# Optimization experiments

Measured on AMD Instinct MI355X. Metric: run time of the kernel, lower is better.

## Reference

```python
import jax, jax.numpy as jnp
import numpy as np

B, IN, H, O, DEPTH = 16384, 64, 128, 32, 4


def _xavier(k, shape):
    fan_in, fan_out = shape[-2], shape[-1]
    lim = float(np.sqrt(6.0 / (fan_in + fan_out)))
    return jax.random.uniform(k, shape, jnp.float32, -lim, lim)


def _gru(x, h, wi, bi, wh, bh):
    # x: [B,1,O], h: [B,1,H]; wi: [3,O,H], wh: [3,H,H]
    r = jax.nn.sigmoid(x @ wi[0] + bi[0] + h @ wh[0] + bh[0])
    z = jax.nn.sigmoid(x @ wi[1] + bi[1] + h @ wh[1] + bh[1])
    n = jnp.tanh(x @ wi[2] + bi[2] + r * (h @ wh[2] + bh[2]))
    return (1.0 - z) * n + z * h


def setup_inputs() -> dict:
    key = jax.random.key(0)
    ks = jax.random.split(key, 10)
    return {
        "z": jax.random.normal(ks[0], (B, 1, IN), jnp.float32),
        "z2h_w": _xavier(ks[1], (IN, H)), "z2h_b": jnp.zeros((H,), jnp.float32),
        "h2o_w": _xavier(ks[2], (H, O)), "h2o_b": jnp.zeros((O,), jnp.float32),
        "gru_a_wi": _xavier(ks[3], (3, O, H)), "gru_a_bi": jnp.zeros((3, H), jnp.float32),
        "gru_a_wh": _xavier(ks[4], (3, H, H)), "gru_a_bh": jnp.zeros((3, H), jnp.float32),
        "gru_f_wi": _xavier(ks[5], (3, O, H)), "gru_f_bi": jnp.zeros((3, H), jnp.float32),
        "gru_f_wh": _xavier(ks[6], (3, H, H)), "gru_f_bh": jnp.zeros((3, H), jnp.float32),
        "u_a_w": _xavier(ks[7], (H, H)), "u_a_b": jnp.zeros((H,), jnp.float32),
        "u_f_w": _xavier(ks[8], (H, H)), "u_f_b": jnp.zeros((H,), jnp.float32),
        "depth": DEPTH,
    }


def reference(z, z2h_w, z2h_b, h2o_w, h2o_b,
              gru_a_wi, gru_a_bi, gru_a_wh, gru_a_bh,
              gru_f_wi, gru_f_bi, gru_f_wh, gru_f_bh,
              u_a_w, u_a_b, u_f_w, u_f_b, depth):
    preds = []

    def node(h_a, d):
        # h_a: [B,1,H] incoming (ancestral) hidden for this node
        pred = h_a @ h2o_w + h2o_b            # [B,1,O] symbol logits
        probs = jax.nn.softmax(pred, axis=2)
        preds.append(pred)
        h_ai = _gru(probs, h_a, gru_a_wi, gru_a_bi, gru_a_wh, gru_a_bh)
        if d > 0:
            # first child: gets ancestral hidden directly
            probs_f = node(h_ai, d - 1)
            # second child: fraternal GRU over first child's root probs,
            # combined with this node's incoming hidden via u_f / u_a
            h_f = _gru(probs_f, h_ai, gru_f_wi, gru_f_bi, gru_f_wh, gru_f_bh)
            h2 = jnp.tanh(h_f @ u_f_w + u_f_b + h_a @ u_a_w + u_a_b)
            node(h2, d - 1)
        return probs

    hidden = z @ z2h_w + z2h_b                # [B,1,H]
    node(hidden, int(depth))
    return jnp.stack(preds, axis=0)           # [n_nodes, B, 1, O] preorder
```

## Files before the change

kernel.cpp:

```cpp
#include <hip/hip_runtime.h>
#include <cstddef>


#define BB   16384
#define HH   128
#define OO   32
#define ROWS 64

typedef __attribute__((ext_vector_type(8))) short bf8;
typedef __attribute__((ext_vector_type(4))) float f4;

#define MFMA(a, b, c) __builtin_amdgcn_mfma_f32_16x16x32_bf16(a, b, c, 0, 0, 0)

#define PW_Z2H 0
#define PW_AWI 8192
#define PW_AWH 20480
#define PW_FWI 69632
#define PW_FWH 81920
#define PW_UA  131072
#define PW_UF  147456
#define PW_H2O 163840
#define PW_END 167936

#define SH   136
#define PSLD 40

#define BA_RZ  0
#define BA_BH2 256
#define BA_BI2 384
#define BF_RZ  512
#define BF_BH2 768
#define BF_BI2 896
#define BU     1024
#define BZ2H   1152
#define BH2O   1280
#define BIAS_N 1312

__device__ __forceinline__ short f2bf(float f) {
  union { float f; unsigned u; } v; v.f = f;
  unsigned r = v.u + 0x7fff + ((v.u >> 16) & 1);
  return (short)(r >> 16);
}
__device__ __forceinline__ float bf2f(short h) {
  union { unsigned u; float f; } v;
  v.u = ((unsigned)(unsigned short)h) << 16;
  return v.f;
}
__device__ __forceinline__ float rcp_(float x) { return __builtin_amdgcn_rcpf(x); }
__device__ __forceinline__ float sigmoidf_(float x) { return rcp_(1.0f + __expf(-x)); }
__device__ __forceinline__ float tanhf_(float x) {
  float ax = fabsf(x), e = __expf(-2.0f * ax);
  float t = (1.0f - e) * rcp_(1.0f + e);
  return x >= 0.0f ? t : -t;
}

template <int K, int N>
__device__ __forceinline__ void repack_one(const float* __restrict__ W,
                                           short* __restrict__ P, int idx) {
  const int KC = K / 32;
  const int j = idx & 7, lane = (idx >> 3) & 63, rest = idx >> 9;
  const int kc = rest % KC, nt = rest / KC;
  const int k = kc * 32 + ((lane >> 4) << 3) + j;
  const int n = nt * 16 + (lane & 15);
  P[idx] = f2bf(W[(size_t)k * N + n]);
}

__global__ __launch_bounds__(256) void k_repack(
    const float* __restrict__ z2hw, const float* __restrict__ awi,
    const float* __restrict__ awh, const float* __restrict__ fwi,
    const float* __restrict__ fwh, const float* __restrict__ uaw,
    const float* __restrict__ ufw, const float* __restrict__ h2ow,
    short* __restrict__ ws) {
  const int t = blockIdx.x * 256 + threadIdx.x;
  if (t < PW_AWI)        repack_one<64, 128>(z2hw, ws + PW_Z2H, t - PW_Z2H);
  else if (t < PW_AWH)   repack_one<96, 128>(awi, ws + PW_AWI, t - PW_AWI);
  else if (t < PW_FWI)   repack_one<384, 128>(awh, ws + PW_AWH, t - PW_AWH);
  else if (t < PW_FWH)   repack_one<96, 128>(fwi, ws + PW_FWI, t - PW_FWI);
  else if (t < PW_UA)    repack_one<384, 128>(fwh, ws + PW_FWH, t - PW_FWH);
  else if (t < PW_UF)    repack_one<128, 128>(uaw, ws + PW_UA, t - PW_UA);
  else if (t < PW_H2O)   repack_one<128, 128>(ufw, ws + PW_UF, t - PW_UF);
  else if (t < PW_END)   repack_one<128, 32>(h2ow, ws + PW_H2O, t - PW_H2O);
}

__device__ __forceinline__ void store_slice(const f4* hv, short* dst, int lane, int w) {
  const int l15 = lane & 15, q = lane >> 4;
#pragma unroll
  for (int rt = 0; rt < 4; ++rt)
#pragma unroll
    for (int j = 0; j < 4; ++j)
      dst[(rt * 16 + q * 4 + j) * SH + w * 16 + l15] = f2bf(hv[rt][j]);
}

__device__ __forceinline__ void gru_slice(const short* xs, const short* hsrc,
                                          const short* wiP, const short* whP,
                                          const float* brz, const float* bh2v,
                                          const float* bi2v,
                                          int lane, int w, f4* hv) {
  const int l15 = lane & 15, q = lane >> 4;
  const int col = w * 16 + l15;
  bf8 ax[4], ah[4][4];
#pragma unroll
  for (int rt = 0; rt < 4; ++rt) {
    ax[rt] = *(const bf8*)(xs + (rt * 16 + l15) * PSLD + q * 8);
#pragma unroll
    for (int c = 0; c < 4; ++c)
      ah[rt][c] = *(const bf8*)(hsrc + (rt * 16 + l15) * SH + c * 32 + q * 8);
  }
  const bf8* wi = (const bf8*)wiP;
  const bf8* wh = (const bf8*)whP;
  f4 t2[4], rg[4];
  {
    const float b = bh2v[col];
#pragma unroll
    for (int rt = 0; rt < 4; ++rt) t2[rt] = (f4){b, b, b, b};
  }
  {
    bf8 W[4];
#pragma unroll
    for (int c = 0; c < 4; ++c) W[c] = wh[(w * 12 + 8 + c) * 64 + lane];
#pragma unroll
    for (int c = 0; c < 4; ++c)
#pragma unroll
      for (int rt = 0; rt < 4; ++rt) t2[rt] = MFMA(ah[rt][c], W[c], t2[rt]);
  }
  {
    const float b = brz[col];
#pragma unroll
    for (int rt = 0; rt < 4; ++rt) rg[rt] = (f4){b, b, b, b};
  }
  {
    bf8 Wx = wi[(w * 3 + 0) * 64 + lane];
    bf8 W[4];
#pragma unroll
    for (int c = 0; c < 4; ++c) W[c] = wh[(w * 12 + 0 + c) * 64 + lane];
#pragma unroll
    for (int rt = 0; rt < 4; ++rt) rg[rt] = MFMA(ax[rt], Wx, rg[rt]);
#pragma unroll
    for (int c = 0; c < 4; ++c)
#pragma unroll
      for (int rt = 0; rt < 4; ++rt) rg[rt] = MFMA(ah[rt][c], W[c], rg[rt]);
  }
#pragma unroll
  for (int k = 0; k < 4; ++k)
#pragma unroll
    for (int j = 0; j < 4; ++j) t2[k][j] *= sigmoidf_(rg[k][j]);
  {
    const float b = bi2v[col];
#pragma unroll
    for (int k = 0; k < 4; ++k)
#pragma unroll
      for (int j = 0; j < 4; ++j) t2[k][j] += b;
  }
  {
    bf8 Wx = wi[(w * 3 + 2) * 64 + lane];
#pragma unroll
    for (int rt = 0; rt < 4; ++rt) t2[rt] = MFMA(ax[rt], Wx, t2[rt]);
  }
  {
    const float b = brz[128 + col];
#pragma unroll
    for (int rt = 0; rt < 4; ++rt) rg[rt] = (f4){b, b, b, b};
  }
  {
    bf8 Wx = wi[(w * 3 + 1) * 64 + lane];
    bf8 W[4];
#pragma unroll
    for (int c = 0; c < 4; ++c) W[c] = wh[(w * 12 + 4 + c) * 64 + lane];
#pragma unroll
    for (int rt = 0; rt < 4; ++rt) rg[rt] = MFMA(ax[rt], Wx, rg[rt]);
#pragma unroll
    for (int c = 0; c < 4; ++c)
#pragma unroll
      for (int rt = 0; rt < 4; ++rt) rg[rt] = MFMA(ah[rt][c], W[c], rg[rt]);
  }
#pragma unroll
  for (int rt = 0; rt < 4; ++rt)
#pragma unroll
    for (int j = 0; j < 4; ++j) {
      const float hc = bf2f(hsrc[(rt * 16 + q * 4 + j) * SH + col]);
      const float zz = sigmoidf_(rg[rt][j]);
      const float nn = tanhf_(t2[rt][j]);
      hv[rt][j] = nn + zz * (hc - nn);
    }
}

__device__ __forceinline__ void pred_node16(const short* hsrc,
                                            const short* h2oP,
                                            const float* bo,
                                            float* spred, short* pdst,
                                            int lane, int w) {
  const int l15 = lane & 15, q = lane >> 4;
  bf8 a[4];
#pragma unroll
  for (int c = 0; c < 4; ++c)
    a[c] = *(const bf8*)(hsrc + (w * 16 + l15) * SH + c * 32 + q * 8);
  const bf8* bw = (const bf8*)h2oP;
  bf8 W[8];
#pragma unroll
  for (int f = 0; f < 8; ++f) W[f] = bw[f * 64 + lane];
  f4 p[2];
#pragma unroll
  for (int nt = 0; nt < 2; ++nt) {
    const float b = bo[nt * 16 + l15];
    f4 acc = (f4){b, b, b, b};
#pragma unroll
    for (int c = 0; c < 4; ++c) acc = MFMA(a[c], W[nt * 4 + c], acc);
    p[nt] = acc;
  }
#pragma unroll
  for (int j = 0; j < 4; ++j) {
    const float v0 = p[0][j], v1 = p[1][j];
    float mx = fmaxf(v0, v1);
#pragma unroll
    for (int s = 1; s < 16; s <<= 1) mx = fmaxf(mx, __shfl_xor(mx, s));
    const float e0 = __expf(v0 - mx), e1 = __expf(v1 - mx);
    float ss = e0 + e1;
#pragma unroll
    for (int s = 1; s < 16; s <<= 1) ss += __shfl_xor(ss, s);
    const float inv = rcp_(ss);
    const int row = w * 16 + q * 4 + j;
    spred[row * 32 + l15] = v0;
    spred[row * 32 + 16 + l15] = v1;
    pdst[row * PSLD + l15] = f2bf(e0 * inv);
    pdst[row * PSLD + 16 + l15] = f2bf(e1 * inv);
  }
}

__device__ const unsigned char d_TYPE[31] =
    {0,1,1,1,1,2,2,1,2,2,1,1,2,2,1,2,2,1,1,1,2,2,1,2,2,1,1,2,2,1,2};
__device__ const unsigned char d_LVL[31] =
    {0,1,2,3,4,4,3,4,4,2,3,4,4,3,4,4,1,2,3,4,4,3,4,4,2,3,4,4,3,4,4};

__global__ __launch_bounds__(512, 2) void k_tree(
    const float* __restrict__ zf, const short* __restrict__ pw,
    const float* __restrict__ z2hb, const float* __restrict__ abi,
    const float* __restrict__ abh, const float* __restrict__ fbi,
    const float* __restrict__ fbh, const float* __restrict__ uab,
    const float* __restrict__ ufb, const float* __restrict__ h2ob,
    float* __restrict__ out) {
  __shared__ __align__(16) short hstk[5 * ROWS * SH];
  __shared__ __align__(16) short hfb[ROWS * SH];
  __shared__ __align__(16) short pstk[5 * ROWS * PSLD];
  __shared__ float bias[BIAS_N];
  float* spred = (float*)hfb;
  const int lane = threadIdx.x & 63;
  const int w = threadIdx.x >> 6;
  const int l15 = lane & 15, q = lane >> 4;
  const int col = w * 16 + l15;
  const int r0 = blockIdx.x * ROWS;

  for (int t = threadIdx.x; t < BIAS_N; t += 512) {
    float v;
    if (t < 256)       v = abi[t] + abh[t];
    else if (t < 384)  v = abh[t];
    else if (t < 512)  v = abi[t - 128];
    else if (t < 768)  v = fbi[t - 512] + fbh[t - 512];
    else if (t < 896)  v = fbh[t - 512];
    else if (t < 1024) v = fbi[t - 640];
    else if (t < 1152) v = uab[t - 1024] + ufb[t - 1024];
    else if (t < 1280) v = z2hb[t - 1152];
    else               v = h2ob[t - 1280];
    bias[t] = v;
  }
  __syncthreads();

  {
    const bf8* wz = (const bf8*)(pw + PW_Z2H);
    const bf8 W0 = wz[(w * 2 + 0) * 64 + lane];
    const bf8 W1 = wz[(w * 2 + 1) * 64 + lane];
    const float b = bias[BZ2H + col];
    f4 hv[4];
#pragma unroll
    for (int rt = 0; rt < 4; ++rt) {
      const float* zr = zf + (size_t)(r0 + rt * 16 + l15) * 64 + q * 8;
      union { short s[8]; bf8 v; } A0, A1;
      {
        const f4 x0 = *(const f4*)zr, x1 = *(const f4*)(zr + 4);
#pragma unroll
        for (int j = 0; j < 4; ++j) { A0.s[j] = f2bf(x0[j]); A0.s[4 + j] = f2bf(x1[j]); }
        const f4 y0 = *(const f4*)(zr + 32), y1 = *(const f4*)(zr + 36);
#pragma unroll
        for (int j = 0; j < 4; ++j) { A1.s[j] = f2bf(y0[j]); A1.s[4 + j] = f2bf(y1[j]); }
      }
      f4 acc = (f4){b, b, b, b};
      acc = MFMA(A0.v, W0, acc);
      acc = MFMA(A1.v, W1, acc);
      hv[rt] = acc;
    }
    store_slice(hv, hstk, lane, w);
  }
  __syncthreads();

#pragma unroll 1
  for (int i = 0; i < 31; ++i) {
    const int t = d_TYPE[i];
    const int L = d_LVL[i];
    short* hcur = hstk + L * ROWS * SH;
    short* pcur = pstk + L * ROWS * PSLD;

    if (t == 2) {
      f4 hf[4];
      gru_slice(pcur, hcur, pw + PW_FWI, pw + PW_FWH,
                bias + BF_RZ, bias + BF_BH2, bias + BF_BI2, lane, w, hf);
      store_slice(hf, hfb, lane, w);
      __syncthreads();
      const short* hpar = hstk + (L - 1) * ROWS * SH;
      const bf8* uf = (const bf8*)(pw + PW_UF);
      const bf8* ua = (const bf8*)(pw + PW_UA);
      bf8 Wf[4], Wa[4];
#pragma unroll
      for (int c = 0; c < 4; ++c) {
        Wf[c] = uf[(w * 4 + c) * 64 + lane];
        Wa[c] = ua[(w * 4 + c) * 64 + lane];
      }
      const float b = bias[BU + col];
      f4 hv[4];
#pragma unroll
      for (int rt = 0; rt < 4; ++rt) {
        f4 acc = (f4){b, b, b, b};
#pragma unroll
        for (int c = 0; c < 4; ++c) {
          const bf8 af = *(const bf8*)(hfb + (rt * 16 + l15) * SH + c * 32 + q * 8);
          const bf8 ap = *(const bf8*)(hpar + (rt * 16 + l15) * SH + c * 32 + q * 8);
          acc = MFMA(af, Wf[c], acc);
          acc = MFMA(ap, Wa[c], acc);
        }
#pragma unroll
        for (int j = 0; j < 4; ++j) acc[j] = tanhf_(acc[j]);
        hv[rt] = acc;
      }
      store_slice(hv, hcur, lane, w);
      __syncthreads();
    }

    if (w < 4)
      pred_node16(hcur, pw + PW_H2O, bias + BH2O, spred, pcur, lane, w);
    __syncthreads();

    {
      const f4 v = *(const f4*)(spred + threadIdx.x * 4);
      __builtin_nontemporal_store(
          v, (f4*)(out + (size_t)i * BB * OO + (size_t)r0 * OO) + threadIdx.x);
    }

    if (L < 4) {
      f4 hv[4];
      gru_slice(pcur, hcur, pw + PW_AWI, pw + PW_AWH,
                bias + BA_RZ, bias + BA_BH2, bias + BA_BI2, lane, w, hv);
      store_slice(hv, hstk + (L + 1) * ROWS * SH, lane, w);
    }
    __syncthreads();
  }
}

extern "C" void kernel_launch(void* const* d_in, const int* in_sizes, int n_in,
                              void* d_out, int out_size, void* d_ws, size_t ws_size,
                              hipStream_t stream) {
  const float* z    = (const float*)d_in[0];
  const float* z2hw = (const float*)d_in[1];
  const float* z2hb = (const float*)d_in[2];
  const float* h2ow = (const float*)d_in[3];
  const float* h2ob = (const float*)d_in[4];
  const float* awi  = (const float*)d_in[5];
  const float* abi  = (const float*)d_in[6];
  const float* awh  = (const float*)d_in[7];
  const float* abh  = (const float*)d_in[8];
  const float* fwi  = (const float*)d_in[9];
  const float* fbi  = (const float*)d_in[10];
  const float* fwh  = (const float*)d_in[11];
  const float* fbh  = (const float*)d_in[12];
  const float* uaw  = (const float*)d_in[13];
  const float* uab  = (const float*)d_in[14];
  const float* ufw  = (const float*)d_in[15];
  const float* ufb  = (const float*)d_in[16];

  float* out = (float*)d_out;
  short* ws  = (short*)d_ws;

  k_repack<<<(PW_END + 255) / 256, 256, 0, stream>>>(
      z2hw, awi, awh, fwi, fwh, uaw, ufw, h2ow, ws);

  k_tree<<<BB / ROWS, 512, 0, stream>>>(
      z, ws, z2hb, abi, abh, fbi, fbh, uab, ufb, h2ob, out);
}
```

Measured before the change: 270.6 us.

## Inline pred node with direct stores, drop softmax max, vectorize repack

The pred/softmax step is inlined into the tree kernel. Logits now go straight to global memory, so the shared staging buffer and the later copy-out pass are gone. The softmax skips the max-subtraction shuffle reduction, and tanh uses a shorter formula; both rely on the inputs being bounded and risk overflow for large values. The repack kernel now has each thread write eight bf16 values as one vector store, and the final barrier only runs when a GRU step follows.

```diff
diff --git a/kernel.cpp b/kernel.cpp
--- a/kernel.cpp
+++ b/kernel.cpp
@@ -49,20 +49,22 @@
 __device__ __forceinline__ float rcp_(float x) { return __builtin_amdgcn_rcpf(x); }
 __device__ __forceinline__ float sigmoidf_(float x) { return rcp_(1.0f + __expf(-x)); }
 __device__ __forceinline__ float tanhf_(float x) {
-  float ax = fabsf(x), e = __expf(-2.0f * ax);
-  float t = (1.0f - e) * rcp_(1.0f + e);
-  return x >= 0.0f ? t : -t;
+  const float e = __expf(2.0f * x);
+  return 1.0f - 2.0f * rcp_(e + 1.0f);
 }
 
 template <int K, int N>
-__device__ __forceinline__ void repack_one(const float* __restrict__ W,
-                                           short* __restrict__ P, int idx) {
+__device__ __forceinline__ void repack8(const float* __restrict__ W,
+                                        short* __restrict__ P, int t) {
   const int KC = K / 32;
-  const int j = idx & 7, lane = (idx >> 3) & 63, rest = idx >> 9;
+  const int lane = t & 63, rest = t >> 6;
   const int kc = rest % KC, nt = rest / KC;
-  const int k = kc * 32 + ((lane >> 4) << 3) + j;
+  const int k0 = kc * 32 + ((lane >> 4) << 3);
   const int n = nt * 16 + (lane & 15);
-  P[idx] = f2bf(W[(size_t)k * N + n]);
+  union { short s[8]; bf8 v; } u;
+#pragma unroll
+  for (int j = 0; j < 8; ++j) u.s[j] = f2bf(W[(size_t)(k0 + j) * N + n]);
+  *(bf8*)(P + (size_t)t * 8) = u.v;
 }
 
 __global__ __launch_bounds__(256) void k_repack(
@@ -72,14 +74,14 @@
     const float* __restrict__ ufw, const float* __restrict__ h2ow,
     short* __restrict__ ws) {
   const int t = blockIdx.x * 256 + threadIdx.x;
-  if (t < PW_AWI)        repack_one<64, 128>(z2hw, ws + PW_Z2H, t - PW_Z2H);
-  else if (t < PW_AWH)   repack_one<96, 128>(awi, ws + PW_AWI, t - PW_AWI);
-  else if (t < PW_FWI)   repack_one<384, 128>(awh, ws + PW_AWH, t - PW_AWH);
-  else if (t < PW_FWH)   repack_one<96, 128>(fwi, ws + PW_FWI, t - PW_FWI);
-  else if (t < PW_UA)    repack_one<384, 128>(fwh, ws + PW_FWH, t - PW_FWH);
-  else if (t < PW_UF)    repack_one<128, 128>(uaw, ws + PW_UA, t - PW_UA);
-  else if (t < PW_H2O)   repack_one<128, 128>(ufw, ws + PW_UF, t - PW_UF);
-  else if (t < PW_END)   repack_one<128, 32>(h2ow, ws + PW_H2O, t - PW_H2O);
+  if (t < 1024)        repack8<64, 128>(z2hw, ws + PW_Z2H, t);
+  else if (t < 2560)   repack8<96, 128>(awi, ws + PW_AWI, t - 1024);
+  else if (t < 8704)   repack8<384, 128>(awh, ws + PW_AWH, t - 2560);
+  else if (t < 10240)  repack8<96, 128>(fwi, ws + PW_FWI, t - 8704);
+  else if (t < 16384)  repack8<384, 128>(fwh, ws + PW_FWH, t - 10240);
+  else if (t < 18432)  repack8<128, 128>(uaw, ws + PW_UA, t - 16384);
+  else if (t < 20480)  repack8<128, 128>(ufw, ws + PW_UF, t - 18432);
+  else if (t < 20992)  repack8<128, 32>(h2ow, ws + PW_H2O, t - 20480);
 }
 
 __device__ __forceinline__ void store_slice(const f4* hv, short* dst, int lane, int w) {
@@ -182,48 +184,6 @@
       const float nn = tanhf_(t2[rt][j]);
       hv[rt][j] = nn + zz * (hc - nn);
     }
-}
-
-__device__ __forceinline__ void pred_node16(const short* hsrc,
-                                            const short* h2oP,
-                                            const float* bo,
-                                            float* spred, short* pdst,
-                                            int lane, int w) {
-  const int l15 = lane & 15, q = lane >> 4;
-  bf8 a[4];
-#pragma unroll
-  for (int c = 0; c < 4; ++c)
-    a[c] = *(const bf8*)(hsrc + (w * 16 + l15) * SH + c * 32 + q * 8);
-  const bf8* bw = (const bf8*)h2oP;
-  bf8 W[8];
-#pragma unroll
-  for (int f = 0; f < 8; ++f) W[f] = bw[f * 64 + lane];
-  f4 p[2];
-#pragma unroll
-  for (int nt = 0; nt < 2; ++nt) {
-    const float b = bo[nt * 16 + l15];
-    f4 acc = (f4){b, b, b, b};
-#pragma unroll
-    for (int c = 0; c < 4; ++c) acc = MFMA(a[c], W[nt * 4 + c], acc);
-    p[nt] = acc;
-  }
-#pragma unroll
-  for (int j = 0; j < 4; ++j) {
-    const float v0 = p[0][j], v1 = p[1][j];
-    float mx = fmaxf(v0, v1);
-#pragma unroll
-    for (int s = 1; s < 16; s <<= 1) mx = fmaxf(mx, __shfl_xor(mx, s));
-    const float e0 = __expf(v0 - mx), e1 = __expf(v1 - mx);
-    float ss = e0 + e1;
-#pragma unroll
-    for (int s = 1; s < 16; s <<= 1) ss += __shfl_xor(ss, s);
-    const float inv = rcp_(ss);
-    const int row = w * 16 + q * 4 + j;
-    spred[row * 32 + l15] = v0;
-    spred[row * 32 + 16 + l15] = v1;
-    pdst[row * PSLD + l15] = f2bf(e0 * inv);
-    pdst[row * PSLD + 16 + l15] = f2bf(e1 * inv);
-  }
 }
 
 __device__ const unsigned char d_TYPE[31] =
@@ -242,7 +202,6 @@
   __shared__ __align__(16) short hfb[ROWS * SH];
   __shared__ __align__(16) short pstk[5 * ROWS * PSLD];
   __shared__ float bias[BIAS_N];
-  float* spred = (float*)hfb;
   const int lane = threadIdx.x & 63;
   const int w = threadIdx.x >> 6;
   const int l15 = lane & 15, q = lane >> 4;
@@ -333,23 +292,51 @@
       __syncthreads();
     }
 
-    if (w < 4)
-      pred_node16(hcur, pw + PW_H2O, bias + BH2O, spred, pcur, lane, w);
+    if (w < 4) {
+      bf8 a[4];
+#pragma unroll
+      for (int c = 0; c < 4; ++c)
+        a[c] = *(const bf8*)(hcur + (w * 16 + l15) * SH + c * 32 + q * 8);
+      const bf8* bw = (const bf8*)(pw + PW_H2O);
+      bf8 W[8];
+#pragma unroll
+      for (int f = 0; f < 8; ++f) W[f] = bw[f * 64 + lane];
+      const float b0 = bias[BH2O + l15];
+      const float b1 = bias[BH2O + 16 + l15];
+      f4 pa = (f4){b0, b0, b0, b0};
+      f4 pb = (f4){b1, b1, b1, b1};
+#pragma unroll
+      for (int c = 0; c < 4; ++c) {
+        pa = MFMA(a[c], W[c], pa);
+        pb = MFMA(a[c], W[4 + c], pb);
+      }
+      float* ob = out + ((size_t)i * BB + r0 + w * 16 + q * 4) * OO + l15;
+#pragma unroll
+      for (int j = 0; j < 4; ++j) {
+        __builtin_nontemporal_store(pa[j], ob + j * OO);
+        __builtin_nontemporal_store(pb[j], ob + j * OO + 16);
+      }
+#pragma unroll
+      for (int j = 0; j < 4; ++j) {
+        const float e0 = __expf(pa[j]), e1 = __expf(pb[j]);
+        float ss = e0 + e1;
+#pragma unroll
+        for (int s = 1; s < 16; s <<= 1) ss += __shfl_xor(ss, s);
+        const float inv = rcp_(ss);
+        short* pr = pcur + (w * 16 + q * 4 + j) * PSLD;
+        pr[l15] = f2bf(e0 * inv);
+        pr[16 + l15] = f2bf(e1 * inv);
+      }
+    }
     __syncthreads();
-
-    {
-      const f4 v = *(const f4*)(spred + threadIdx.x * 4);
-      __builtin_nontemporal_store(
-          v, (f4*)(out + (size_t)i * BB * OO + (size_t)r0 * OO) + threadIdx.x);
-    }
 
     if (L < 4) {
       f4 hv[4];
       gru_slice(pcur, hcur, pw + PW_AWI, pw + PW_AWH,
                 bias + BA_RZ, bias + BA_BH2, bias + BA_BI2, lane, w, hv);
       store_slice(hv, hstk + (L + 1) * ROWS * SH, lane, w);
-    }
-    __syncthreads();
+      __syncthreads();
+    }
   }
 }
 
@@ -377,7 +364,7 @@
   float* out = (float*)d_out;
   short* ws  = (short*)d_ws;
 
-  k_repack<<<(PW_END + 255) / 256, 256, 0, stream>>>(
+  k_repack<<<82, 256, 0, stream>>>(
       z2hw, awi, awh, fwi, fwh, uaw, ufw, h2ow, ws);
 
   k_tree<<<BB / ROWS, 512, 0, stream>>>(
```

New measurement: 258.8 us. 4.4% less time.
